# Performance work log

Measured on AMD Instinct MI355X. Metric: run time of the kernel, lower is better.

The kernel has to match this reference:

```python
import jax, jax.numpy as jnp
import numpy as np
import math

L = 4          # num_layers
NH = 8         # num_heads
EPS = 1e-5


def _mha(x, Wqkv, bqkv, Wo, bo):
    # x: (S, B, D). Faithful to torch nn.MultiheadAttention (eval mode).
    S, B, D = x.shape
    hd = D // NH
    qkv = jnp.einsum('sbd,ed->sbe', x, Wqkv) + bqkv            # (S,B,3D)
    q, k, v = jnp.split(qkv, 3, axis=-1)
    def heads(t):
        return t.reshape(S, B, NH, hd).transpose(1, 2, 0, 3)   # (B,H,S,hd)
    q, k, v = heads(q), heads(k), heads(v)
    scale = 1.0 / math.sqrt(hd)
    att = jax.nn.softmax(jnp.einsum('bhqd,bhkd->bhqk', q * scale, k), axis=-1)
    o = jnp.einsum('bhqk,bhkd->bhqd', att, v)                  # (B,H,S,hd)
    o = o.transpose(2, 0, 1, 3).reshape(S, B, D)
    return o @ Wo.T + bo


def _layer_norm(x, g, b):
    mu = jnp.mean(x, axis=-1, keepdims=True)
    var = jnp.var(x, axis=-1, keepdims=True)
    return (x - mu) / jnp.sqrt(var + EPS) * g + b


def _pos_encoding(S, D, dtype):
    pos = jnp.arange(S, dtype=jnp.float32)[:, None]
    div = jnp.exp(jnp.arange(0, D, 2, dtype=jnp.float32) * (-math.log(10000.0) / D))
    pe = jnp.stack([jnp.sin(pos * div), jnp.cos(pos * div)], axis=-1).reshape(S, D)
    return pe.astype(dtype)


def setup_inputs() -> dict:
    key = jax.random.key(0)
    B, S, IN, D, OUT = 8, 2048, 14, 512, 1
    FF = 4 * D
    ks = iter(jax.random.split(key, 32))
    s = 0.02
    inp = {
        'x': jax.random.normal(next(ks), (B, S, IN), jnp.float32),
        'W_emb': jax.random.normal(next(ks), (D, IN), jnp.float32) * s,
        'b_emb': jnp.zeros((D,), jnp.float32),
        'Wqkv_g': jax.random.normal(next(ks), (L, 3 * D, D), jnp.float32) * s,
        'bqkv_g': jnp.zeros((L, 3 * D), jnp.float32),
        'Wo_g': jax.random.normal(next(ks), (L, D, D), jnp.float32) * s,
        'bo_g': jnp.zeros((L, D), jnp.float32),
        'Wqkv_l': jax.random.normal(next(ks), (L, 3 * D, D), jnp.float32) * s,
        'bqkv_l': jnp.zeros((L, 3 * D), jnp.float32),
        'Wo_l': jax.random.normal(next(ks), (L, D, D), jnp.float32) * s,
        'bo_l': jnp.zeros((L, D), jnp.float32),
        'W1': jax.random.normal(next(ks), (L, FF, D), jnp.float32) * s,
        'b1f': jnp.zeros((L, FF), jnp.float32),
        'W2': jax.random.normal(next(ks), (L, D, FF), jnp.float32) * s,
        'b2f': jnp.zeros((L, D), jnp.float32),
        'g1': jnp.ones((L, D), jnp.float32),
        'be1': jnp.zeros((L, D), jnp.float32),
        'g2': jnp.ones((L, D), jnp.float32),
        'be2': jnp.zeros((L, D), jnp.float32),
        'W_out': jax.random.normal(next(ks), (OUT, D), jnp.float32) * s,
        'b_out': jnp.zeros((OUT,), jnp.float32),
    }
    return inp


def reference(x, W_emb, b_emb, Wqkv_g, bqkv_g, Wo_g, bo_g, Wqkv_l, bqkv_l,
              Wo_l, bo_l, W1, b1f, W2, b2f, g1, be1, g2, be2, W_out, b_out):
    B, S, _ = x.shape
    D = W_emb.shape[0]
    h = x @ W_emb.T + b_emb                       # (B,S,D)
    h = h + _pos_encoding(S, D, h.dtype)[None]
    h = h.transpose(1, 0, 2)                      # (S,B,D)

    w = max(1, S // 4)                            # local window size
    nw = S // w                                   # S divisible by w here
    for i in range(L):
        g_out = _mha(h, Wqkv_g[i], bqkv_g[i], Wo_g[i], bo_g[i])
        # local windows: fold window index into batch (attention is per-batch)
        xl = h.reshape(nw, w, B, D).transpose(1, 0, 2, 3).reshape(w, nw * B, D)
        l_out = _mha(xl, Wqkv_l[i], bqkv_l[i], Wo_l[i], bo_l[i])
        l_out = l_out.reshape(w, nw, B, D).transpose(1, 0, 2, 3).reshape(S, B, D)
        h = _layer_norm(h + g_out + l_out, g1[i], be1[i])
        ff = jax.nn.relu(h @ W1[i].T + b1f[i]) @ W2[i].T + b2f[i]
        h = _layer_norm(h + ff, g2[i], be2[i])

    return h[-1] @ W_out.T + b_out                # (B, output_dim)
```

## Files before the change

### kernel.cpp

```cpp
#include <hip/hip_runtime.h>
#include <hip/hip_bf16.h>

#define DEV __device__ __forceinline__

typedef __attribute__((ext_vector_type(4))) float f32x4;
typedef __attribute__((ext_vector_type(8))) short s16x8;
typedef unsigned short u16;

constexpr int Bsz = 8;
constexpr int S   = 2048;
constexpr int Dm  = 512;
constexpr int NHd = 8;
constexpr int FFd = 2048;
constexpr int Ln  = 4;
constexpr int T   = S * Bsz;

DEV u16 f2bf(float f) {
  union { float f; unsigned u; } v; v.f = f;
  unsigned r = v.u + 0x7fff + ((v.u >> 16) & 1);
  return (u16)(r >> 16);
}
DEV float bf2f(u16 a) { union { unsigned u; float f; } v; v.u = ((unsigned)a) << 16; return v.f; }
DEV float exp2g(float x) { return __builtin_amdgcn_exp2f(x); }

typedef __attribute__((address_space(1))) const unsigned int guint;
typedef __attribute__((address_space(3))) unsigned int luint;
DEV void gload16(const void* g, void* l) {
  __builtin_amdgcn_global_load_lds((guint*)g, (luint*)l, 16, 0, 0);
}

__global__ void cvt_bf16_kernel(const float* __restrict__ src, u16* __restrict__ dst, int n4) {
  int i = (blockIdx.x * 256 + threadIdx.x);
  if (i >= n4) return;
  float4 v = *reinterpret_cast<const float4*>(src + i * 4);
  ushort4 o; o.x = f2bf(v.x); o.y = f2bf(v.y); o.z = f2bf(v.z); o.w = f2bf(v.w);
  *reinterpret_cast<ushort4*>(dst + i * 4) = o;
}

__global__ void cvt_wo_kernel(const float* __restrict__ g, const float* __restrict__ l,
                              u16* __restrict__ dst) {
  int i = blockIdx.x * 256 + threadIdx.x;
  int e = i * 4;
  int li = e >> 19;
  int rem = e & 524287;
  int n = rem >> 10, k = rem & 1023;
  const float* src = (k < 512) ? (g + ((size_t)li * 512 + n) * 512 + k)
                               : (l + ((size_t)li * 512 + n) * 512 + (k - 512));
  float4 v = *reinterpret_cast<const float4*>(src);
  ushort4 o; o.x = f2bf(v.x); o.y = f2bf(v.y); o.z = f2bf(v.z); o.w = f2bf(v.w);
  *reinterpret_cast<ushort4*>(dst + e) = o;
}

__global__ void embed_kernel(const float* __restrict__ x, const float* __restrict__ Wemb,
                             const float* __restrict__ bemb, float* __restrict__ hf,
                             u16* __restrict__ hb) {
  int t = blockIdx.x;
  int b = t >> 11, s = t & 2047;
  const float* xr = x + ((size_t)b * S + s) * 14;
  float xv[14];
  #pragma unroll
  for (int i = 0; i < 14; i++) xv[i] = xr[i];
  for (int d = threadIdx.x; d < Dm; d += blockDim.x) {
    const float* wr = Wemb + d * 14;
    float acc = bemb[d];
    #pragma unroll
    for (int i = 0; i < 14; i++) acc += xv[i] * wr[i];
    float ang = (float)s * expf((float)((d >> 1) * 2) * (-9.210340371976184f / 512.0f));
    acc += (d & 1) ? cosf(ang) : sinf(ang);
    hf[(size_t)t * Dm + d] = acc;
    hb[(size_t)t * Dm + d] = f2bf(acc);
  }
}

template<int OMODE, int VPACK, int BSUM>
__global__ __launch_bounds__(256, 3)
void gemm_bt_kernel(const u16* __restrict__ A, const u16* __restrict__ Bt,
                    const float* __restrict__ bias1, const float* __restrict__ bias2,
                    void* __restrict__ Cout, u16* __restrict__ vpk,
                    int M, int N, int K) {
  __shared__ __align__(16) u16 As[2][128 * 32];
  __shared__ __align__(16) u16 Bs[2][128 * 32];
  const int tid = threadIdx.x;
  const int lane = tid & 63, w = tid >> 6;
  const int wr = w >> 1, wc = w & 1;
  const int lr = lane & 15, lg = lane >> 4;
  const int m0 = blockIdx.y * 128, n0 = blockIdx.x * 128;

  f32x4 acc[4][4] = {};

  const int c1 = tid, c2 = tid + 256;
  const u16* gA1 = A + (size_t)(m0 + (c1 >> 2)) * K + (c1 & 3) * 8;
  const u16* gA2 = A + (size_t)(m0 + (c2 >> 2)) * K + (c2 & 3) * 8;
  const u16* gB1 = Bt + (size_t)(n0 + (c1 >> 2)) * K + (c1 & 3) * 8;
  const u16* gB2 = Bt + (size_t)(n0 + (c2 >> 2)) * K + (c2 & 3) * 8;

  const int nk = K >> 5;
  auto stage = [&](int t, int c) {
    const int kt = t * 32;
    gload16(gA1 + kt, As[c] + c1 * 8); gload16(gA2 + kt, As[c] + c2 * 8);
    gload16(gB1 + kt, Bs[c] + c1 * 8); gload16(gB2 + kt, Bs[c] + c2 * 8);
  };

  stage(0, 0);
  for (int t = 0; t < nk; ++t) {
    const int c = t & 1;
    if (t + 1 < nk) {
      stage(t + 1, c ^ 1);
      asm volatile("s_waitcnt vmcnt(4)" ::: "memory");
    } else {
      asm volatile("s_waitcnt vmcnt(0)" ::: "memory");
    }
    __builtin_amdgcn_s_barrier();

    s16x8 a[4], bb[4];
    #pragma unroll
    for (int i = 0; i < 4; i++) {
      a[i]  = *reinterpret_cast<const s16x8*>(As[c] + ((wr * 64 + i * 16 + lr) * 32 + lg * 8));
      bb[i] = *reinterpret_cast<const s16x8*>(Bs[c] + ((wc * 64 + i * 16 + lr) * 32 + lg * 8));
    }
    #pragma unroll
    for (int mi = 0; mi < 4; mi++)
      #pragma unroll
      for (int ni = 0; ni < 4; ni++)
        acc[mi][ni] = __builtin_amdgcn_mfma_f32_16x16x32_bf16(a[mi], bb[ni], acc[mi][ni], 0, 0, 0);

    __builtin_amdgcn_s_barrier();
  }

  const int sec = VPACK ? (n0 >> 9) : 0;
  const bool isv = VPACK && (sec == 2 || sec == 5);
  const int ldc = VPACK ? 2048 : N;
  const int csub = (VPACK && sec >= 3) ? 512 : 0;
  u16* vdst = nullptr;
  if (isv) vdst = vpk + (sec == 5 ? 8388608 : 0);

  #pragma unroll
  for (int mi = 0; mi < 4; mi++) {
    int row = m0 + wr * 64 + mi * 16 + lg * 4;
    #pragma unroll
    for (int ni = 0; ni < 4; ni++) {
      int col = n0 + wc * 64 + ni * 16 + lr;
      float bv;
      if (VPACK)      bv = (col < 1536) ? bias1[col] : bias2[col - 1536];
      else if (BSUM)  bv = bias1[col] + bias2[col];
      else            bv = bias1[col];
      if (isv) {
        int vcol = col - (sec == 2 ? 1024 : 2560);
        int hh = vcol >> 6, dd = vcol & 63;
        int bb2 = row >> 11, ss = row & 2047;
        ushort4 o;
        o.x = f2bf(acc[mi][ni][0] + bv);
        o.y = f2bf(acc[mi][ni][1] + bv);
        o.z = f2bf(acc[mi][ni][2] + bv);
        o.w = f2bf(acc[mi][ni][3] + bv);
        *reinterpret_cast<ushort4*>(vdst + ((size_t)(bb2 * NHd + hh) * 64 + dd) * S + ss) = o;
      } else {
        #pragma unroll
        for (int r = 0; r < 4; r++) {
          float v = acc[mi][ni][r] + bv;
          if (OMODE == 2) v = v > 0.f ? v : 0.f;
          ((u16*)Cout)[(size_t)(row + r) * ldc + (col - csub)] = f2bf(v);
        }
      }
    }
  }
}

__global__ __launch_bounds__(256, 3)
void flash_kernel(const u16* __restrict__ qkv, const u16* __restrict__ vpk_all,
                  u16* __restrict__ ctx) {
  const int tid = threadIdx.x;
  const int lane = tid & 63, w = tid >> 6;
  const int lr = lane & 15, lg = lane >> 4;
  const int bid = blockIdx.x;
  const int half = bid >> 10;
  const int bid10 = bid & 1023;
  const int h = bid10 & 7;
  const int r_ = bid10 >> 3;
  const int S_att = half ? 512 : 2048;
  const int lognqb = half ? 2 : 4;
  const int qb = r_ & ((1 << lognqb) - 1);
  const int cw = r_ >> lognqb;
  const int b = cw & 7, n = cw >> 3;
  const int qoff = half ? 1024 : 0;
  const int koff = half ? 1536 : 512;
  const int coff = half ? 512 : 0;
  const u16* v_pk = vpk_all + (half ? 8388608 : 0);
  const int s_base = n * S_att;
  const int q0A = qb * 128 + w * 16;
  const int q0B = q0A + 64;

  __shared__ __align__(16) u16 KT[2][4096];
  __shared__ __align__(16) u16 VT[2][4096];
  __shared__ __align__(16) u16 p_lds_all[4][2][16][72];
  u16 (*p_ldsA)[72] = p_lds_all[w][0];
  u16 (*p_ldsB)[72] = p_lds_all[w][1];

  const u16* vbase = v_pk + (size_t)(b * NHd + h) * 64 * S + s_base;

  s16x8 qfA[2], qfB[2];
  {
    const float qs = 0.18033688011112042f;
    const u16* qpA = qkv + ((size_t)b * S + s_base + q0A + lr) * 2048 + qoff + h * 64 + lg * 8;
    const u16* qpB = qkv + ((size_t)b * S + s_base + q0B + lr) * 2048 + qoff + h * 64 + lg * 8;
    s16x8 a0 = *reinterpret_cast<const s16x8*>(qpA);
    s16x8 a1 = *reinterpret_cast<const s16x8*>(qpA + 32);
    s16x8 b0 = *reinterpret_cast<const s16x8*>(qpB);
    s16x8 b1 = *reinterpret_cast<const s16x8*>(qpB + 32);
    #pragma unroll
    for (int j = 0; j < 8; j++) {
      qfA[0][j] = (short)f2bf(bf2f((u16)a0[j]) * qs);
      qfA[1][j] = (short)f2bf(bf2f((u16)a1[j]) * qs);
      qfB[0][j] = (short)f2bf(bf2f((u16)b0[j]) * qs);
      qfB[1][j] = (short)f2bf(bf2f((u16)b1[j]) * qs);
    }
  }

  s16x8 ones;
  #pragma unroll
  for (int j = 0; j < 8; j++) ones[j] = (short)0x3F80;

  float mA = -1e30f, mB = -1e30f;
  f32x4 laccA = (f32x4){0.f, 0.f, 0.f, 0.f}, laccB = (f32x4){0.f, 0.f, 0.f, 0.f};
  f32x4 oaccA[4], oaccB[4];
  #pragma unroll
  for (int nt = 0; nt < 4; nt++) {
    oaccA[nt] = (f32x4){0.f, 0.f, 0.f, 0.f};
    oaccB[nt] = (f32x4){0.f, 0.f, 0.f, 0.f};
  }

  const int seg = tid & 7, sr1 = tid >> 3, sr2 = (tid >> 3) + 32;
  const int ssw1 = (seg ^ (sr1 & 7)) * 8, ssw2 = (seg ^ (sr2 & 7)) * 8;

  const u16* kroot = qkv + ((size_t)b * S + s_base) * 2048 + koff + h * 64;

  auto stage = [&](int kb, int c) {
    const u16* kt = kroot + (size_t)kb * 2048;
    gload16(kt + (size_t)sr1 * 2048 + ssw1, &KT[c][tid * 8]);
    gload16(kt + (size_t)sr2 * 2048 + ssw2, &KT[c][2048 + tid * 8]);
    const u16* vt = vbase + kb;
    gload16(vt + (size_t)sr1 * S + ssw1, &VT[c][tid * 8]);
    gload16(vt + (size_t)sr2 * S + ssw2, &VT[c][2048 + tid * 8]);
  };

  stage(0, 0);
  __syncthreads();

  for (int kb = 0; kb < S_att; kb += 64) {
    const int c = (kb >> 6) & 1;
    if (kb + 64 < S_att) stage(kb + 64, c ^ 1);

    f32x4 sgA[4], sgB[4];
    __builtin_amdgcn_s_setprio(1);
    #pragma unroll
    for (int g = 0; g < 4; g++) {
      const int key = g * 16 + lr, kw = key & 7;
      const u16* kp = &KT[c][key * 64];
      s16x8 k0 = *reinterpret_cast<const s16x8*>(kp + ((lg ^ kw) * 8));
      s16x8 k1 = *reinterpret_cast<const s16x8*>(kp + (((4 + lg) ^ kw) * 8));
      f32x4 sa = (f32x4){0.f, 0.f, 0.f, 0.f};
      sa = __builtin_amdgcn_mfma_f32_16x16x32_bf16(k0, qfA[0], sa, 0, 0, 0);
      sa = __builtin_amdgcn_mfma_f32_16x16x32_bf16(k1, qfA[1], sa, 0, 0, 0);
      sgA[g] = sa;
      f32x4 sb = (f32x4){0.f, 0.f, 0.f, 0.f};
      sb = __builtin_amdgcn_mfma_f32_16x16x32_bf16(k0, qfB[0], sb, 0, 0, 0);
      sb = __builtin_amdgcn_mfma_f32_16x16x32_bf16(k1, qfB[1], sb, 0, 0, 0);
      sgB[g] = sb;
    }
    __builtin_amdgcn_s_setprio(0);

    float tmA, tmB;
    {
      float t0 = fmaxf(fmaxf(sgA[0][0], sgA[0][1]), fmaxf(sgA[0][2], sgA[0][3]));
      float t1 = fmaxf(fmaxf(sgA[1][0], sgA[1][1]), fmaxf(sgA[1][2], sgA[1][3]));
      float t2 = fmaxf(fmaxf(sgA[2][0], sgA[2][1]), fmaxf(sgA[2][2], sgA[2][3]));
      float t3 = fmaxf(fmaxf(sgA[3][0], sgA[3][1]), fmaxf(sgA[3][2], sgA[3][3]));
      tmA = fmaxf(fmaxf(t0, t1), fmaxf(t2, t3));
      tmA = fmaxf(tmA, __shfl_xor(tmA, 16, 64));
      tmA = fmaxf(tmA, __shfl_xor(tmA, 32, 64));
      float u0 = fmaxf(fmaxf(sgB[0][0], sgB[0][1]), fmaxf(sgB[0][2], sgB[0][3]));
      float u1 = fmaxf(fmaxf(sgB[1][0], sgB[1][1]), fmaxf(sgB[1][2], sgB[1][3]));
      float u2 = fmaxf(fmaxf(sgB[2][0], sgB[2][1]), fmaxf(sgB[2][2], sgB[2][3]));
      float u3 = fmaxf(fmaxf(sgB[3][0], sgB[3][1]), fmaxf(sgB[3][2], sgB[3][3]));
      tmB = fmaxf(fmaxf(u0, u1), fmaxf(u2, u3));
      tmB = fmaxf(tmB, __shfl_xor(tmB, 16, 64));
      tmB = fmaxf(tmB, __shfl_xor(tmB, 32, 64));
    }
    if (__any((int)(tmA > mA + 8.f))) {
      float mnew = fmaxf(mA, tmA);
      float cf = exp2g(mA - mnew);
      mA = mnew;
      #pragma unroll
      for (int r = 0; r < 4; r++) {
        float co = __shfl(cf, lg * 4 + r, 16);
        laccA[r] *= co;
        #pragma unroll
        for (int nt = 0; nt < 4; nt++) oaccA[nt][r] *= co;
      }
    }
    if (__any((int)(tmB > mB + 8.f))) {
      float mnew = fmaxf(mB, tmB);
      float cf = exp2g(mB - mnew);
      mB = mnew;
      #pragma unroll
      for (int r = 0; r < 4; r++) {
        float co = __shfl(cf, lg * 4 + r, 16);
        laccB[r] *= co;
        #pragma unroll
        for (int nt = 0; nt < 4; nt++) oaccB[nt][r] *= co;
      }
    }

    #pragma unroll
    for (int g = 0; g < 4; g++) {
      float e0 = exp2g(sgA[g][0] - mA);
      float e1 = exp2g(sgA[g][1] - mA);
      float e2 = exp2g(sgA[g][2] - mA);
      float e3 = exp2g(sgA[g][3] - mA);
      unsigned p01, p23;
      asm("v_cvt_pk_bf16_f32 %0, %1, %2" : "=v"(p01) : "v"(e0), "v"(e1));
      asm("v_cvt_pk_bf16_f32 %0, %1, %2" : "=v"(p23) : "v"(e2), "v"(e3));
      uint2 pk; pk.x = p01; pk.y = p23;
      *reinterpret_cast<uint2*>(&p_ldsA[lr][g * 16 + lg * 4]) = pk;
    }
    #pragma unroll
    for (int g = 0; g < 4; g++) {
      float e0 = exp2g(sgB[g][0] - mB);
      float e1 = exp2g(sgB[g][1] - mB);
      float e2 = exp2g(sgB[g][2] - mB);
      float e3 = exp2g(sgB[g][3] - mB);
      unsigned p01, p23;
      asm("v_cvt_pk_bf16_f32 %0, %1, %2" : "=v"(p01) : "v"(e0), "v"(e1));
      asm("v_cvt_pk_bf16_f32 %0, %1, %2" : "=v"(p23) : "v"(e2), "v"(e3));
      uint2 pk; pk.x = p01; pk.y = p23;
      *reinterpret_cast<uint2*>(&p_ldsB[lr][g * 16 + lg * 4]) = pk;
    }
    asm volatile("s_waitcnt lgkmcnt(0)" ::: "memory");

    __builtin_amdgcn_s_setprio(1);
    #pragma unroll
    for (int kc = 0; kc < 2; kc++) {
      s16x8 paA = *reinterpret_cast<const s16x8*>(&p_ldsA[lr][kc * 32 + lg * 8]);
      s16x8 paB = *reinterpret_cast<const s16x8*>(&p_ldsB[lr][kc * 32 + lg * 8]);
      laccA = __builtin_amdgcn_mfma_f32_16x16x32_bf16(paA, ones, laccA, 0, 0, 0);
      laccB = __builtin_amdgcn_mfma_f32_16x16x32_bf16(paB, ones, laccB, 0, 0, 0);
      #pragma unroll
      for (int nt = 0; nt < 4; nt++) {
        const int d = nt * 16 + lr;
        s16x8 vfr = *reinterpret_cast<const s16x8*>(
            &VT[c][d * 64 + (((kc * 4 + lg) ^ (d & 7)) * 8)]);
        oaccA[nt] = __builtin_amdgcn_mfma_f32_16x16x32_bf16(paA, vfr, oaccA[nt], 0, 0, 0);
        oaccB[nt] = __builtin_amdgcn_mfma_f32_16x16x32_bf16(paB, vfr, oaccB[nt], 0, 0, 0);
      }
    }
    __builtin_amdgcn_s_setprio(0);

    __syncthreads();
  }

  #pragma unroll
  for (int nt = 0; nt < 4; nt++)
    #pragma unroll
    for (int r = 0; r < 4; r++) {
      float vA = oaccA[nt][r] / laccA[r];
      size_t tqA = (size_t)b * S + s_base + q0A + lg * 4 + r;
      ctx[tqA * 1024 + coff + h * 64 + nt * 16 + lr] = f2bf(vA);
      float vB = oaccB[nt][r] / laccB[r];
      size_t tqB = (size_t)b * S + s_base + q0B + lg * 4 + r;
      ctx[tqB * 1024 + coff + h * 64 + nt * 16 + lr] = f2bf(vB);
    }
}

template<int NADD>
__global__ void ln_kernel(const float* __restrict__ hin, const u16* __restrict__ a1,
                          const u16* __restrict__ a2, const float* __restrict__ gamma,
                          const float* __restrict__ beta, float* __restrict__ hf,
                          u16* __restrict__ hb) {
  int row = blockIdx.x * 4 + (threadIdx.x >> 6);
  int lane = threadIdx.x & 63;
  size_t base = (size_t)row * 512 + lane * 8;
  float4 h0 = *reinterpret_cast<const float4*>(hin + base);
  float4 h1 = *reinterpret_cast<const float4*>(hin + base + 4);
  s16x8 x1 = *reinterpret_cast<const s16x8*>(a1 + base);
  s16x8 x2 = {};
  if (NADD == 2) x2 = *reinterpret_cast<const s16x8*>(a2 + base);
  float v[8];
  float hv[8] = {h0.x, h0.y, h0.z, h0.w, h1.x, h1.y, h1.z, h1.w};
  float sum = 0.f;
  #pragma unroll
  for (int j = 0; j < 8; j++) {
    float t = hv[j] + bf2f((u16)x1[j]);
    if (NADD == 2) t += bf2f((u16)x2[j]);
    v[j] = t; sum += t;
  }
  #pragma unroll
  for (int o = 32; o >= 1; o >>= 1) sum += __shfl_xor(sum, o, 64);
  float mean = sum * (1.0f / 512.0f);
  float sq = 0.f;
  #pragma unroll
  for (int j = 0; j < 8; j++) { float d = v[j] - mean; sq += d * d; }
  #pragma unroll
  for (int o = 32; o >= 1; o >>= 1) sq += __shfl_xor(sq, o, 64);
  float rstd = rsqrtf(sq * (1.0f / 512.0f) + 1e-5f);
  #pragma unroll
  for (int j = 0; j < 8; j++) {
    int d = lane * 8 + j;
    float o = (v[j] - mean) * rstd * gamma[d] + beta[d];
    hf[base + j] = o;
    hb[base + j] = f2bf(o);
  }
}

__global__ void out_kernel(const float* __restrict__ hf, const float* __restrict__ Wout,
                           const float* __restrict__ bout, float* __restrict__ out) {
  int b = blockIdx.x; int lane = threadIdx.x;
  size_t base = ((size_t)b * S + S - 1) * 512;
  float s = 0.f;
  #pragma unroll
  for (int j = 0; j < 8; j++) { int d = lane * 8 + j; s += hf[base + d] * Wout[d]; }
  #pragma unroll
  for (int o = 32; o >= 1; o >>= 1) s += __shfl_xor(s, o, 64);
  if (lane == 0) out[b] = s + bout[0];
}

extern "C" void kernel_launch(void* const* d_in, const int* in_sizes, int n_in,
                              void* d_out, int out_size, void* d_ws, size_t ws_size,
                              hipStream_t stream) {
  (void)in_sizes; (void)n_in; (void)out_size; (void)ws_size;
  const float* x      = (const float*)d_in[0];
  const float* W_emb  = (const float*)d_in[1];
  const float* b_emb  = (const float*)d_in[2];
  const float* Wqkv_g = (const float*)d_in[3];
  const float* bqkv_g = (const float*)d_in[4];
  const float* Wo_g   = (const float*)d_in[5];
  const float* bo_g   = (const float*)d_in[6];
  const float* Wqkv_l = (const float*)d_in[7];
  const float* bqkv_l = (const float*)d_in[8];
  const float* Wo_l   = (const float*)d_in[9];
  const float* bo_l   = (const float*)d_in[10];
  const float* W1     = (const float*)d_in[11];
  const float* b1f    = (const float*)d_in[12];
  const float* W2     = (const float*)d_in[13];
  const float* b2f    = (const float*)d_in[14];
  const float* g1     = (const float*)d_in[15];
  const float* be1    = (const float*)d_in[16];
  const float* g2     = (const float*)d_in[17];
  const float* be2    = (const float*)d_in[18];
  const float* W_out  = (const float*)d_in[19];
  const float* b_out  = (const float*)d_in[20];
  float* out = (float*)d_out;

  char* ws = (char*)d_ws;
  u16*   w_bf = (u16*)ws;
  float* h_f  = (float*)(ws + 33554432);
  u16*   h_b  = (u16*)(ws + 67108864);
  u16*   qkv  = (u16*)(ws + 83886080);
  u16*   ff1  = (u16*)(ws + 83886080);
  u16*   vpk  = (u16*)(ws + 150994944);
  u16*   ctx  = (u16*)(ws + 184549376);
  u16*   go   = (u16*)(ws + 218103808);

  u16* wqkvF = w_bf;
  u16* woF   = w_bf + 6291456;
  u16* w1b   = w_bf + 8388608;
  u16* w2b   = w_bf + 12582912;

  auto cvt = [&](const float* s_, u16* d_, int n) {
    cvt_bf16_kernel<<<(n / 4 + 255) / 256, 256, 0, stream>>>(s_, d_, n / 4);
  };
  for (int i = 0; i < Ln; i++) {
    cvt(Wqkv_g + (size_t)i * 786432, wqkvF + (size_t)i * 1572864, 786432);
    cvt(Wqkv_l + (size_t)i * 786432, wqkvF + (size_t)i * 1572864 + 786432, 786432);
  }
  cvt_wo_kernel<<<2048, 256, 0, stream>>>(Wo_g, Wo_l, woF);
  cvt(W1, w1b, 4194304);
  cvt(W2, w2b, 4194304);

  embed_kernel<<<T, 256, 0, stream>>>(x, W_emb, b_emb, h_f, h_b);

  for (int i = 0; i < Ln; i++) {
    gemm_bt_kernel<1, 1, 0><<<dim3(3072 / 128, T / 128), 256, 0, stream>>>(
        h_b, wqkvF + (size_t)i * 1572864, bqkv_g + i * 1536, bqkv_l + i * 1536,
        qkv, vpk, T, 3072, 512);
    flash_kernel<<<dim3(2048), 256, 0, stream>>>(qkv, vpk, ctx);
    gemm_bt_kernel<1, 0, 1><<<dim3(512 / 128, T / 128), 256, 0, stream>>>(
        ctx, woF + (size_t)i * 524288, bo_g + i * 512, bo_l + i * 512,
        go, nullptr, T, 512, 1024);
    ln_kernel<1><<<T / 4, 256, 0, stream>>>(h_f, go, nullptr, g1 + i * 512, be1 + i * 512, h_f, h_b);
    gemm_bt_kernel<2, 0, 0><<<dim3(FFd / 128, T / 128), 256, 0, stream>>>(
        h_b, w1b + (size_t)i * 1048576, b1f + i * 2048, nullptr, ff1, nullptr, T, 2048, 512);
    gemm_bt_kernel<1, 0, 0><<<dim3(512 / 128, T / 128), 256, 0, stream>>>(
        ff1, w2b + (size_t)i * 1048576, b2f + i * 512, nullptr, go, nullptr, T, 512, 2048);
    ln_kernel<1><<<T / 4, 256, 0, stream>>>(h_f, go, nullptr, g2 + i * 512, be2 + i * 512, h_f, h_b);
  }

  out_kernel<<<Bsz, 64, 0, stream>>>(h_f, W_out, b_out, out);
}
```

Measured before the change: 1.548 ms.

## Single-buffer flash K/V tiles via register staging and raise occupancy to 4

The flash attention kernel drops its double-buffered LDS tiles for K and V filled by direct global-to-LDS loads. It now prefetches the next tile into registers during compute and writes it to a single LDS buffer after an extra barrier. Launch bounds are raised to 4 blocks per CU, made possible by the smaller LDS footprint, and the row-max reduction is rewritten as a linear chain. The trade-off is an extra __syncthreads per iteration and more register pressure from the staging registers, which may cause spills under the tighter bound.

```diff
diff --git a/kernel.cpp b/kernel.cpp
--- a/kernel.cpp
+++ b/kernel.cpp
@@ -166,7 +166,7 @@
   }
 }
 
-__global__ __launch_bounds__(256, 3)
+__global__ __launch_bounds__(256, 4)
 void flash_kernel(const u16* __restrict__ qkv, const u16* __restrict__ vpk_all,
                   u16* __restrict__ ctx) {
   const int tid = threadIdx.x;
@@ -190,8 +190,8 @@
   const int q0A = qb * 128 + w * 16;
   const int q0B = q0A + 64;
 
-  __shared__ __align__(16) u16 KT[2][4096];
-  __shared__ __align__(16) u16 VT[2][4096];
+  __shared__ __align__(16) u16 KT[4096];
+  __shared__ __align__(16) u16 VT[4096];
   __shared__ __align__(16) u16 p_lds_all[4][2][16][72];
   u16 (*p_ldsA)[72] = p_lds_all[w][0];
   u16 (*p_ldsB)[72] = p_lds_all[w][1];
@@ -234,28 +234,36 @@
 
   const u16* kroot = qkv + ((size_t)b * S + s_base) * 2048 + koff + h * 64;
 
-  auto stage = [&](int kb, int c) {
+  s16x8 stg[4];
+  auto load = [&](int kb) {
     const u16* kt = kroot + (size_t)kb * 2048;
-    gload16(kt + (size_t)sr1 * 2048 + ssw1, &KT[c][tid * 8]);
-    gload16(kt + (size_t)sr2 * 2048 + ssw2, &KT[c][2048 + tid * 8]);
+    stg[0] = *reinterpret_cast<const s16x8*>(kt + (size_t)sr1 * 2048 + ssw1);
+    stg[1] = *reinterpret_cast<const s16x8*>(kt + (size_t)sr2 * 2048 + ssw2);
     const u16* vt = vbase + kb;
-    gload16(vt + (size_t)sr1 * S + ssw1, &VT[c][tid * 8]);
-    gload16(vt + (size_t)sr2 * S + ssw2, &VT[c][2048 + tid * 8]);
+    stg[2] = *reinterpret_cast<const s16x8*>(vt + (size_t)sr1 * S + ssw1);
+    stg[3] = *reinterpret_cast<const s16x8*>(vt + (size_t)sr2 * S + ssw2);
   };
-
-  stage(0, 0);
+  auto commit = [&]() {
+    *reinterpret_cast<s16x8*>(&KT[tid * 8]) = stg[0];
+    *reinterpret_cast<s16x8*>(&KT[2048 + tid * 8]) = stg[1];
+    *reinterpret_cast<s16x8*>(&VT[tid * 8]) = stg[2];
+    *reinterpret_cast<s16x8*>(&VT[2048 + tid * 8]) = stg[3];
+  };
+
+  load(0);
+  commit();
   __syncthreads();
 
   for (int kb = 0; kb < S_att; kb += 64) {
-    const int c = (kb >> 6) & 1;
-    if (kb + 64 < S_att) stage(kb + 64, c ^ 1);
+    const bool more = kb + 64 < S_att;
+    if (more) load(kb + 64);
 
     f32x4 sgA[4], sgB[4];
     __builtin_amdgcn_s_setprio(1);
     #pragma unroll
     for (int g = 0; g < 4; g++) {
       const int key = g * 16 + lr, kw = key & 7;
-      const u16* kp = &KT[c][key * 64];
+      const u16* kp = &KT[key * 64];
       s16x8 k0 = *reinterpret_cast<const s16x8*>(kp + ((lg ^ kw) * 8));
       s16x8 k1 = *reinterpret_cast<const s16x8*>(kp + (((4 + lg) ^ kw) * 8));
       f32x4 sa = (f32x4){0.f, 0.f, 0.f, 0.f};
@@ -271,20 +279,26 @@
 
     float tmA, tmB;
     {
-      float t0 = fmaxf(fmaxf(sgA[0][0], sgA[0][1]), fmaxf(sgA[0][2], sgA[0][3]));
-      float t1 = fmaxf(fmaxf(sgA[1][0], sgA[1][1]), fmaxf(sgA[1][2], sgA[1][3]));
-      float t2 = fmaxf(fmaxf(sgA[2][0], sgA[2][1]), fmaxf(sgA[2][2], sgA[2][3]));
-      float t3 = fmaxf(fmaxf(sgA[3][0], sgA[3][1]), fmaxf(sgA[3][2], sgA[3][3]));
-      tmA = fmaxf(fmaxf(t0, t1), fmaxf(t2, t3));
-      tmA = fmaxf(tmA, __shfl_xor(tmA, 16, 64));
-      tmA = fmaxf(tmA, __shfl_xor(tmA, 32, 64));
-      float u0 = fmaxf(fmaxf(sgB[0][0], sgB[0][1]), fmaxf(sgB[0][2], sgB[0][3]));
-      float u1 = fmaxf(fmaxf(sgB[1][0], sgB[1][1]), fmaxf(sgB[1][2], sgB[1][3]));
-      float u2 = fmaxf(fmaxf(sgB[2][0], sgB[2][1]), fmaxf(sgB[2][2], sgB[2][3]));
-      float u3 = fmaxf(fmaxf(sgB[3][0], sgB[3][1]), fmaxf(sgB[3][2], sgB[3][3]));
-      tmB = fmaxf(fmaxf(u0, u1), fmaxf(u2, u3));
-      tmB = fmaxf(tmB, __shfl_xor(tmB, 16, 64));
-      tmB = fmaxf(tmB, __shfl_xor(tmB, 32, 64));
+      float m_ = fmaxf(sgA[0][0], sgA[0][1]);
+      m_ = fmaxf(fmaxf(m_, sgA[0][2]), sgA[0][3]);
+      m_ = fmaxf(fmaxf(m_, sgA[1][0]), sgA[1][1]);
+      m_ = fmaxf(fmaxf(m_, sgA[1][2]), sgA[1][3]);
+      m_ = fmaxf(fmaxf(m_, sgA[2][0]), sgA[2][1]);
+      m_ = fmaxf(fmaxf(m_, sgA[2][2]), sgA[2][3]);
+      m_ = fmaxf(fmaxf(m_, sgA[3][0]), sgA[3][1]);
+      m_ = fmaxf(fmaxf(m_, sgA[3][2]), sgA[3][3]);
+      m_ = fmaxf(m_, __shfl_xor(m_, 16, 64));
+      tmA = fmaxf(m_, __shfl_xor(m_, 32, 64));
+      float u_ = fmaxf(sgB[0][0], sgB[0][1]);
+      u_ = fmaxf(fmaxf(u_, sgB[0][2]), sgB[0][3]);
+      u_ = fmaxf(fmaxf(u_, sgB[1][0]), sgB[1][1]);
+      u_ = fmaxf(fmaxf(u_, sgB[1][2]), sgB[1][3]);
+      u_ = fmaxf(fmaxf(u_, sgB[2][0]), sgB[2][1]);
+      u_ = fmaxf(fmaxf(u_, sgB[2][2]), sgB[2][3]);
+      u_ = fmaxf(fmaxf(u_, sgB[3][0]), sgB[3][1]);
+      u_ = fmaxf(fmaxf(u_, sgB[3][2]), sgB[3][3]);
+      u_ = fmaxf(u_, __shfl_xor(u_, 16, 64));
+      tmB = fmaxf(u_, __shfl_xor(u_, 32, 64));
     }
     if (__any((int)(tmA > mA + 8.f))) {
       float mnew = fmaxf(mA, tmA);
@@ -348,13 +362,15 @@
       for (int nt = 0; nt < 4; nt++) {
         const int d = nt * 16 + lr;
         s16x8 vfr = *reinterpret_cast<const s16x8*>(
-            &VT[c][d * 64 + (((kc * 4 + lg) ^ (d & 7)) * 8)]);
+            &VT[d * 64 + (((kc * 4 + lg) ^ (d & 7)) * 8)]);
         oaccA[nt] = __builtin_amdgcn_mfma_f32_16x16x32_bf16(paA, vfr, oaccA[nt], 0, 0, 0);
         oaccB[nt] = __builtin_amdgcn_mfma_f32_16x16x32_bf16(paB, vfr, oaccB[nt], 0, 0, 0);
       }
     }
     __builtin_amdgcn_s_setprio(0);
 
+    __syncthreads();
+    if (more) commit();
     __syncthreads();
   }
 
```

Result: slower. 1.710 ms (+10.5%).
